# Optimization experiments

Measured on AMD Instinct MI355X. Metric: run time of the kernel, lower is better.

The kernel has to match this reference:

```python
import jax, jax.numpy as jnp
import numpy as np

B, L, D, H = 8, 1024, 1024, 16
DPH = D // H  # 64


def setup_inputs() -> dict:
    key = jax.random.key(0)
    ks = jax.random.split(key, 12)
    s = 1.0 / np.sqrt(D)
    return {
        "key": jax.random.normal(ks[0], (B, L, D), jnp.float32),
        "value": jax.random.normal(ks[1], (B, L, D), jnp.float32),
        "query": jax.random.normal(ks[2], (B, L, D), jnp.float32),
        "attn_mask": jax.random.randint(ks[3], (B, L, L), 0, 2) > 0,
        "Wq": jax.random.normal(ks[4], (D, D), jnp.float32) * s,
        "bq": jnp.zeros((D,), jnp.float32),
        "Wk": jax.random.normal(ks[5], (D, D), jnp.float32) * s,
        "bk": jnp.zeros((D,), jnp.float32),
        "Wv": jax.random.normal(ks[6], (D, D), jnp.float32) * s,
        "bv": jnp.zeros((D,), jnp.float32),
        "Wo": jax.random.normal(ks[7], (D, D), jnp.float32) * s,
        "bo": jnp.zeros((D,), jnp.float32),
        "gamma": jnp.ones((D,), jnp.float32),
        "beta": jnp.zeros((D,), jnp.float32),
    }


def _layer_norm(x, gamma, beta, eps=1e-5):
    mu = jnp.mean(x, axis=-1, keepdims=True)
    var = jnp.var(x, axis=-1, keepdims=True)
    return (x - mu) * jax.lax.rsqrt(var + eps) * gamma + beta


def reference(key, value, query, attn_mask, Wq, bq, Wk, bk, Wv, bv, Wo, bo, gamma, beta):
    residual = query
    k = key @ Wk + bk      # [B, L, D]
    v = value @ Wv + bv
    q = query @ Wq + bq
    # faithful to torch: raw row-major view into [B*H, L, dph] (NOT standard head transpose)
    k = k.reshape(B * H, -1, DPH)
    v = v.reshape(B * H, -1, DPH)
    q = q.reshape(B * H, -1, DPH)
    # faithful to torch repeat: tile whole batch H times along dim 0
    mask = jnp.tile(attn_mask, (H, 1, 1))  # [B*H, L, L]
    scale = DPH ** (-0.5)
    scores = jnp.einsum('bqd,bkd->bqk', q, k) * scale
    scores = jnp.where(mask, jnp.float32(-1e9), scores)
    attention = jax.nn.softmax(scores, axis=2)
    context = jnp.einsum('bqk,bkd->bqd', attention, v)  # [B*H, L, dph]
    context = context.reshape(B, -1, D)
    output = context @ Wo + bo
    output = _layer_norm(residual + output, gamma, beta)
    return (output, attention)
```

## Files before the change

kernel.cpp:

```cpp
#include <hip/hip_runtime.h>

typedef __attribute__((ext_vector_type(8))) short short8;
typedef __attribute__((ext_vector_type(4))) float f32x4;

#define AS1C(p) ((const __attribute__((address_space(1))) void*)(p))
#define AS3(p)  ((__attribute__((address_space(3))) void*)(p))

__device__ __forceinline__ unsigned short f2bf(float f) {
  unsigned int u = __float_as_uint(f);
  return (unsigned short)((u + 0x7fffu + ((u >> 16) & 1u)) >> 16);
}

__device__ __forceinline__ void gload16(const void* g, void* l) {
  __builtin_amdgcn_global_load_lds(AS1C(g), AS3(l), 16, 0, 0);
}

#define EXP_C 0.18033688011112042f

__global__ __launch_bounds__(256) void prep_kernel(const float* __restrict__ W0,
                                                   const float* __restrict__ W1,
                                                   const float* __restrict__ W2,
                                                   const float* __restrict__ W3,
                                                   unsigned short* __restrict__ WtBase,
                                                   const int* __restrict__ m,
                                                   unsigned int* __restrict__ bitsT,
                                                   const float* __restrict__ s0,
                                                   const float* __restrict__ s1,
                                                   const float* __restrict__ s2,
                                                   unsigned short* __restrict__ d0,
                                                   unsigned short* __restrict__ d1,
                                                   unsigned short* __restrict__ d2) {
  int bid = blockIdx.x;
  if (bid < 4096) {
    __shared__ float t[32][33];
    int z = bid >> 10;
    int rb = bid & 1023;
    int bx = (rb & 31) * 32, by = (rb >> 5) * 32;
    const float* W = (z == 0) ? W0 : (z == 1) ? W1 : (z == 2) ? W2 : W3;
    unsigned short* Wt = WtBase + (size_t)z * 1024 * 1024;
    int tx = threadIdx.x & 31, ty = threadIdx.x >> 5;
#pragma unroll
    for (int i = 0; i < 4; ++i) {
      int r = ty + i * 8;
      t[r][tx] = W[(size_t)(by + r) * 1024 + bx + tx];
    }
    __syncthreads();
#pragma unroll
    for (int i = 0; i < 4; ++i) {
      int r = ty + i * 8;
      Wt[(size_t)(bx + r) * 1024 + by + tx] = f2bf(t[tx][r]);
    }
  } else if (bid < 36864) {
    int i = (bid - 4096) * 256 + threadIdx.x;
    unsigned long long bl = __ballot(m[i] != 0);
    if ((threadIdx.x & 63) == 0) {
      int b_ = i >> 20, q = (i >> 10) & 1023, k = i & 1023;
      int w = k >> 5;
      bitsT[b_ * 32768 + w * 1024 + q]       = (unsigned int)bl;
      bitsT[b_ * 32768 + (w + 1) * 1024 + q] = (unsigned int)(bl >> 32);
    }
  } else {
    int cb = bid - 36864;
    int z = cb >> 13;
    const float* in = (z == 0) ? s0 : (z == 1) ? s1 : s2;
    unsigned short* out = (z == 0) ? d0 : (z == 1) ? d1 : d2;
    int i = (cb & 8191) * 256 + threadIdx.x;
    float4 v = ((const float4*)in)[i];
    ushort4 o;
    o.x = f2bf(v.x); o.y = f2bf(v.y); o.z = f2bf(v.z); o.w = f2bf(v.w);
    ((ushort4*)out)[i] = o;
  }
}

__global__ __launch_bounds__(256) void conv_bf16(const float* __restrict__ in,
                                                 unsigned short* __restrict__ out, int n4) {
  int i = blockIdx.x * 256 + threadIdx.x;
  if (i >= n4) return;
  float4 v = ((const float4*)in)[i];
  ushort4 o;
  o.x = f2bf(v.x); o.y = f2bf(v.y); o.z = f2bf(v.z); o.w = f2bf(v.w);
  ((ushort4*)out)[i] = o;
}

__global__ __launch_bounds__(256) void transpose_v(const unsigned short* __restrict__ v,
                                                   unsigned short* __restrict__ vt) {
  __shared__ unsigned short t[32][33];
  int b = blockIdx.z;
  int bx = blockIdx.x * 32;
  int by = blockIdx.y * 32;
  int tx = threadIdx.x & 31, ty = threadIdx.x >> 5;
#pragma unroll
  for (int i = 0; i < 4; ++i) {
    int r = ty + i * 8;
    t[r][tx] = v[(size_t)b * 65536 + (size_t)(by + r) * 64 + bx + tx];
  }
  __syncthreads();
#pragma unroll
  for (int i = 0; i < 4; ++i) {
    int r = ty + i * 8;
    vt[(size_t)b * 65536 + (size_t)(bx + r) * 1024 + by + tx] = t[tx][r];
  }
}

template <int MODE>
__device__ __forceinline__ void gemm_body(
    const unsigned short* __restrict__ A, const unsigned short* __restrict__ Bt,
    const float* __restrict__ bias, const float* __restrict__ res,
    unsigned short* __restrict__ Cb, float* __restrict__ Cf,
    unsigned short* lA, unsigned short* lB) {
  const int K = 1024, N = 1024;
  const int tid = threadIdx.x;
  const int wave = tid >> 6, lane = tid & 63;
  const int row_l = lane & 15, kg = lane >> 4;
  const int wg = blockIdx.y * 8 + blockIdx.x;
  const int idx = (wg & 7) * 64 + (wg >> 3);
  const int m0 = (idx >> 3) * 128, n0 = (idx & 7) * 128;
  const int wm = (wave >> 1) * 64, wn = (wave & 1) * 64;
  f32x4 acc[4][4] = {};

  for (int k0 = 0; k0 < K; k0 += 64) {
    __syncthreads();
#pragma unroll
    for (int it = 0; it < 4; ++it) {
      int c = wave * 64 + it * 256 + lane;
      int r = c >> 3, ch = c & 7;
      int sch = ch ^ (r & 7);
      gload16(A + (size_t)(m0 + r) * K + k0 + sch * 8, lA + (wave * 64 + it * 256) * 8);
      gload16(Bt + (size_t)(n0 + r) * K + k0 + sch * 8, lB + (wave * 64 + it * 256) * 8);
    }
    __syncthreads();
#pragma unroll
    for (int kk = 0; kk < 2; ++kk) {
      short8 af[4], bfr[4];
#pragma unroll
      for (int t = 0; t < 4; ++t) {
        int ra = wm + t * 16 + row_l;
        af[t] = *(const short8*)(lA + ra * 64 + (((kk * 4 + kg) ^ (ra & 7)) << 3));
        int rb = wn + t * 16 + row_l;
        bfr[t] = *(const short8*)(lB + rb * 64 + (((kk * 4 + kg) ^ (rb & 7)) << 3));
      }
      __builtin_amdgcn_s_setprio(1);
#pragma unroll
      for (int mt = 0; mt < 4; ++mt)
#pragma unroll
        for (int nt = 0; nt < 4; ++nt)
          acc[mt][nt] = __builtin_amdgcn_mfma_f32_16x16x32_bf16(af[mt], bfr[nt], acc[mt][nt], 0, 0, 0);
      __builtin_amdgcn_s_setprio(0);
    }
  }
#pragma unroll
  for (int mt = 0; mt < 4; ++mt)
#pragma unroll
    for (int nt = 0; nt < 4; ++nt)
#pragma unroll
      for (int r = 0; r < 4; ++r) {
        int grow = m0 + wm + mt * 16 + kg * 4 + r;
        int gcol = n0 + wn + nt * 16 + row_l;
        float v = acc[mt][nt][r] + bias[gcol];
        if (MODE == 0) {
          Cb[(size_t)grow * N + gcol] = f2bf(v);
        } else {
          v += res[(size_t)grow * N + gcol];
          Cf[(size_t)grow * N + gcol] = v;
        }
      }
}

__global__ __launch_bounds__(256) void gemm_qkv_kernel(
    const unsigned short* __restrict__ A0, const unsigned short* __restrict__ A1,
    const unsigned short* __restrict__ A2, const unsigned short* __restrict__ WtBase,
    const float* __restrict__ b0, const float* __restrict__ b1, const float* __restrict__ b2,
    unsigned short* __restrict__ C0, unsigned short* __restrict__ C1,
    unsigned short* __restrict__ C2) {
  __shared__ unsigned short lA[128 * 64];
  __shared__ unsigned short lB[128 * 64];
  int z = blockIdx.z;
  const unsigned short* A = (z == 0) ? A0 : (z == 1) ? A1 : A2;
  const float* bias = (z == 0) ? b0 : (z == 1) ? b1 : b2;
  unsigned short* C = (z == 0) ? C0 : (z == 1) ? C1 : C2;
  gemm_body<0>(A, WtBase + (size_t)z * 1024 * 1024, bias, nullptr, C, nullptr, lA, lB);
}

__global__ __launch_bounds__(256) void gemm_out_kernel(
    const unsigned short* __restrict__ A, const unsigned short* __restrict__ Bt,
    const float* __restrict__ bias, const float* __restrict__ res, float* __restrict__ Cf) {
  __shared__ unsigned short lA[128 * 64];
  __shared__ unsigned short lB[128 * 64];
  gemm_body<1>(A, Bt, bias, res, nullptr, Cf, lA, lB);
}

__global__ __launch_bounds__(256) void attn_kernel(
    const unsigned short* __restrict__ Q,
    const unsigned short* __restrict__ Km,
    const unsigned short* __restrict__ Vt,
    const unsigned int* __restrict__ mbitsT,
    float* __restrict__ attn,
    unsigned short* __restrict__ ctx) {
  __shared__ unsigned short lQ[64 * 64];
  __shared__ unsigned short lK[64 * 64];
  __shared__ unsigned short lV[64 * 64];
  const int tid = threadIdx.x, wave = tid >> 6, lane = tid & 63;
  const int row_l = lane & 15, kg = lane >> 4;
  const int wg = blockIdx.y * 16 + blockIdx.x;
  const int idx = (wg & 7) * 256 + (wg >> 3);
  const int batch = idx >> 4, qt = idx & 15;
  const int q0 = qt * 64;
  const unsigned short* Qb = Q + (size_t)batch * 65536;
  const unsigned short* Kb = Km + (size_t)batch * 65536;
  const unsigned short* Vb = Vt + (size_t)batch * 65536;
  const unsigned int* mT = mbitsT + (size_t)(batch & 7) * 32768;
  float* attb = attn + (size_t)batch * 1048576;
  const int q_loc = wave * 16 + row_l;
  const int q_lane = q0 + q_loc;

#define STAGE_K_TO(kt, dst)                                                           \
  {                                                                                   \
    _Pragma("unroll") for (int it = 0; it < 2; ++it) {                                \
      int c = wave * 64 + it * 256 + lane;                                            \
      int r_ = c >> 3, ch_ = c & 7, sch_ = ch_ ^ (r_ & 7);                            \
      gload16(Kb + (size_t)((kt) * 64 + r_) * 64 + sch_ * 8,                          \
              (dst) + (wave * 64 + it * 256) * 8);                                    \
    }                                                                                 \
  }
#define STAGE_V_TO(kt, dst)                                                           \
  {                                                                                   \
    _Pragma("unroll") for (int it = 0; it < 2; ++it) {                                \
      int c = wave * 64 + it * 256 + lane;                                            \
      int r_ = c >> 3, ch_ = c & 7, sch_ = ch_ ^ (r_ & 7);                            \
      gload16(Vb + (size_t)r_ * 1024 + (kt) * 64 + sch_ * 8,                          \
              (dst) + (wave * 64 + it * 256) * 8);                                    \
    }                                                                                 \
  }
#define WAIT_BAR0                                             \
  asm volatile("s_waitcnt vmcnt(0)" ::: "memory");            \
  __builtin_amdgcn_s_barrier();

#pragma unroll
  for (int it = 0; it < 2; ++it) {
    int c = wave * 64 + it * 256 + lane;
    int r = c >> 3, ch = c & 7;
    int sch = ch ^ (r & 7);
    gload16(Qb + (size_t)(q0 + r) * 64 + sch * 8, lQ + (wave * 64 + it * 256) * 8);
  }
  STAGE_K_TO(0, lK)
  WAIT_BAR0
  short8 qf[2];
#pragma unroll
  for (int kk = 0; kk < 2; ++kk)
    qf[kk] = *(const short8*)(lQ + q_loc * 64 + (((kk * 4 + kg) ^ (q_loc & 7)) << 3));

  float l_part = 0.f;

  auto pass1_step = [&](const unsigned short* kbuf, int kt) {
    unsigned int mw0 = mT[(kt * 2 + 0) * 1024 + q_lane];
    unsigned int mw1 = mT[(kt * 2 + 1) * 1024 + q_lane];
    f32x4 s[4];
    __builtin_amdgcn_s_setprio(1);
#pragma unroll
    for (int cf = 0; cf < 4; ++cf) {
      int rk = cf * 16 + row_l;
      f32x4 a = {0.f, 0.f, 0.f, 0.f};
#pragma unroll
      for (int kk = 0; kk < 2; ++kk) {
        short8 kf = *(const short8*)(kbuf + rk * 64 + (((kk * 4 + kg) ^ (rk & 7)) << 3));
        a = __builtin_amdgcn_mfma_f32_16x16x32_bf16(kf, qf[kk], a, 0, 0, 0);
      }
      s[cf] = a;
    }
    __builtin_amdgcn_s_setprio(0);
#pragma unroll
    for (int cf = 0; cf < 4; ++cf) {
      unsigned int w = (cf < 2) ? mw0 : mw1;
#pragma unroll
      for (int r = 0; r < 4; ++r) {
        int bit = (w >> ((cf & 1) * 16 + kg * 4 + r)) & 1;
        float e = __builtin_exp2f(s[cf][r] * EXP_C);
        l_part += bit ? 0.f : e;
      }
    }
  };
  for (int kt2 = 0; kt2 < 16; kt2 += 2) {
    STAGE_K_TO(kt2 + 1, lV)
    pass1_step(lK, kt2);
    WAIT_BAR0
    if (kt2 + 2 < 16) STAGE_K_TO(kt2 + 2, lK)
    pass1_step(lV, kt2 + 1);
    WAIT_BAR0
  }
  float se = l_part;
  se += __shfl_xor(se, 16);
  se += __shfl_xor(se, 32);
  const float il = 1.f / se;

  f32x4 cacc[4] = {};
  unsigned short* lP = lQ;

  for (int kt = 0; kt < 16; ++kt) {
    __syncthreads();
    STAGE_K_TO(kt, lK)
    STAGE_V_TO(kt, lV)
    WAIT_BAR0
    unsigned int mw0 = mT[(kt * 2 + 0) * 1024 + q_lane];
    unsigned int mw1 = mT[(kt * 2 + 1) * 1024 + q_lane];
    f32x4 s[4];
    __builtin_amdgcn_s_setprio(1);
#pragma unroll
    for (int cf = 0; cf < 4; ++cf) {
      int rk = cf * 16 + row_l;
      f32x4 a = {0.f, 0.f, 0.f, 0.f};
#pragma unroll
      for (int kk = 0; kk < 2; ++kk) {
        short8 kf = *(const short8*)(lK + rk * 64 + (((kk * 4 + kg) ^ (rk & 7)) << 3));
        a = __builtin_amdgcn_mfma_f32_16x16x32_bf16(kf, qf[kk], a, 0, 0, 0);
      }
      s[cf] = a;
    }
    __builtin_amdgcn_s_setprio(0);
#pragma unroll
    for (int cf = 0; cf < 4; ++cf) {
      unsigned int w = (cf < 2) ? mw0 : mw1;
      f32x4 o;
      unsigned short pb[4];
#pragma unroll
      for (int r = 0; r < 4; ++r) {
        int bit = (w >> ((cf & 1) * 16 + kg * 4 + r)) & 1;
        float p = bit ? 0.f : __builtin_exp2f(s[cf][r] * EXP_C) * il;
        o[r] = p;
        pb[r] = f2bf(p);
      }
      int swc = (cf * 2 + (kg >> 1)) ^ (q_loc & 7);
      *(uint2*)((char*)lP + q_loc * 128 + swc * 16 + (kg & 1) * 8) = *(const uint2*)pb;
      __builtin_nontemporal_store(
          o, (f32x4*)(attb + (size_t)q_lane * 1024 + kt * 64 + cf * 16 + kg * 4));
    }
    __builtin_amdgcn_s_setprio(1);
#pragma unroll
    for (int kk = 0; kk < 2; ++kk) {
      short8 pa = *(const short8*)(lP + q_loc * 64 + (((kk * 4 + kg) ^ (q_loc & 7)) << 3));
#pragma unroll
      for (int df = 0; df < 4; ++df) {
        int rv = df * 16 + row_l;
        short8 vb = *(const short8*)(lV + rv * 64 + (((kk * 4 + kg) ^ (rv & 7)) << 3));
        cacc[df] = __builtin_amdgcn_mfma_f32_16x16x32_bf16(pa, vb, cacc[df], 0, 0, 0);
      }
    }
    __builtin_amdgcn_s_setprio(0);
  }
#pragma unroll
  for (int df = 0; df < 4; ++df)
#pragma unroll
    for (int r = 0; r < 4; ++r) {
      int grow = q0 + wave * 16 + kg * 4 + r;
      int gcol = df * 16 + row_l;
      ctx[(size_t)batch * 65536 + (size_t)grow * 64 + gcol] = f2bf(cacc[df][r]);
    }
#undef STAGE_K_TO
#undef STAGE_V_TO
#undef WAIT_BAR0
}

__global__ __launch_bounds__(256) void layernorm_kernel(float* __restrict__ io,
                                                        const float* __restrict__ gamma,
                                                        const float* __restrict__ beta) {
  int wave = threadIdx.x >> 6, lane = threadIdx.x & 63;
  size_t row = (size_t)blockIdx.x * 4 + wave;
  float* p = io + row * 1024;
  float4 v[4];
  float s = 0.f, ss = 0.f;
#pragma unroll
  for (int i = 0; i < 4; ++i) {
    v[i] = ((const float4*)p)[lane + i * 64];
    s += v[i].x + v[i].y + v[i].z + v[i].w;
    ss += v[i].x * v[i].x + v[i].y * v[i].y + v[i].z * v[i].z + v[i].w * v[i].w;
  }
#pragma unroll
  for (int m = 1; m < 64; m <<= 1) { s += __shfl_xor(s, m); ss += __shfl_xor(ss, m); }
  float mu = s * (1.f / 1024.f);
  float var = ss * (1.f / 1024.f) - mu * mu;
  float rinv = rsqrtf(var + 1e-5f);
#pragma unroll
  for (int i = 0; i < 4; ++i) {
    int idx = lane + i * 64;
    float4 g = ((const float4*)gamma)[idx];
    float4 b = ((const float4*)beta)[idx];
    float4 o;
    o.x = (v[i].x - mu) * rinv * g.x + b.x;
    o.y = (v[i].y - mu) * rinv * g.y + b.y;
    o.z = (v[i].z - mu) * rinv * g.z + b.z;
    o.w = (v[i].w - mu) * rinv * g.w + b.w;
    ((float4*)p)[idx] = o;
  }
}

extern "C" void kernel_launch(void* const* d_in, const int* in_sizes, int n_in,
                              void* d_out, int out_size, void* d_ws, size_t ws_size,
                              hipStream_t stream) {
  const float* key   = (const float*)d_in[0];
  const float* value = (const float*)d_in[1];
  const float* query = (const float*)d_in[2];
  const int* amask   = (const int*)d_in[3];
  const float* Wq = (const float*)d_in[4];
  const float* bq = (const float*)d_in[5];
  const float* Wk = (const float*)d_in[6];
  const float* bk = (const float*)d_in[7];
  const float* Wv = (const float*)d_in[8];
  const float* bv = (const float*)d_in[9];
  const float* Wo = (const float*)d_in[10];
  const float* bo = (const float*)d_in[11];
  const float* gamma = (const float*)d_in[12];
  const float* beta  = (const float*)d_in[13];

  char* ws = (char*)d_ws;
  const size_t MB = 1024 * 1024;
  float* out_f = (float*)d_out;
  float* attn_f = (float*)d_out + (size_t)8388608;
  const int n4 = 8388608 / 4;
  dim3 gemm_grid(8, 64);
  dim3 gemm_grid3(8, 64, 3);
  dim3 attn_grid(16, 128);

  const bool big_ws = ws_size >= 106 * MB;
  if (big_ws) {
    unsigned short* A0 = (unsigned short*)(ws + 0);
    unsigned short* A1 = (unsigned short*)(ws + 16 * MB);
    unsigned short* A2 = (unsigned short*)(ws + 32 * MB);
    unsigned short* B1 = (unsigned short*)(ws + 48 * MB);
    unsigned short* B2 = (unsigned short*)(ws + 64 * MB);
    unsigned short* B3 = (unsigned short*)(ws + 80 * MB);
    unsigned short* Wts = (unsigned short*)(ws + 96 * MB);
    unsigned int* mbitsT = (unsigned int*)(ws + 104 * MB);

    prep_kernel<<<61440, 256, 0, stream>>>(Wq, Wk, Wv, Wo, Wts, amask, mbitsT,
                                           query, key, value, A0, A1, A2);
    gemm_qkv_kernel<<<gemm_grid3, 256, 0, stream>>>(A0, A1, A2, Wts, bq, bk, bv, B1, B2, B3);
    transpose_v<<<dim3(2, 32, 128), 256, 0, stream>>>(B3, A1);
    attn_kernel<<<attn_grid, 256, 0, stream>>>(B1, B2, A1, mbitsT, attn_f, A2);
    gemm_out_kernel<<<gemm_grid, 256, 0, stream>>>(A2, Wts + 3 * MB, bo, query, out_f);
    layernorm_kernel<<<2048, 256, 0, stream>>>(out_f, gamma, beta);
  } else {
    unsigned short* B0 = (unsigned short*)(ws + 0);
    unsigned short* B1 = (unsigned short*)(ws + 16 * MB);
    unsigned short* B2 = (unsigned short*)(ws + 32 * MB);
    unsigned short* B3 = (unsigned short*)(ws + 48 * MB);
    unsigned short* Wts = (unsigned short*)(ws + 64 * MB);
    unsigned int* mbitsT = (unsigned int*)(ws + 72 * MB);

    prep_kernel<<<36864, 256, 0, stream>>>(Wq, Wk, Wv, Wo, Wts, amask, mbitsT,
                                           query, key, value, B0, B0, B0);
    conv_bf16<<<8192, 256, 0, stream>>>(query, B0, n4);
    gemm_qkv_kernel<<<gemm_grid, 256, 0, stream>>>(B0, B0, B0, Wts, bq, bq, bq, B1, B1, B1);
    conv_bf16<<<8192, 256, 0, stream>>>(key, B0, n4);
    gemm_qkv_kernel<<<gemm_grid, 256, 0, stream>>>(B0, B0, B0, Wts + 1 * MB, bk, bk, bk, B2, B2, B2);
    conv_bf16<<<8192, 256, 0, stream>>>(value, B0, n4);
    gemm_qkv_kernel<<<gemm_grid, 256, 0, stream>>>(B0, B0, B0, Wts + 2 * MB, bv, bv, bv, B3, B3, B3);
    transpose_v<<<dim3(2, 32, 128), 256, 0, stream>>>(B3, B0);
    attn_kernel<<<attn_grid, 256, 0, stream>>>(B1, B2, B0, mbitsT, attn_f, B3);
    gemm_out_kernel<<<gemm_grid, 256, 0, stream>>>(B3, Wts + 3 * MB, bo, query, out_f);
    layernorm_kernel<<<2048, 256, 0, stream>>>(out_f, gamma, beta);
  }
}
```

Before: 321.6 us.

## Process two query tiles per attention block, fusing tile B's row-sum pass into tile A's output pass

Each attention workgroup now handles 128 queries as two 64-row sub-tiles that share the same K/V staging, and the grid is halved to match. The row-sum pass for sub-tile B runs inside sub-tile A's output loop, so K is streamed three times per 128 queries instead of four. The pass-1 K loop also loses its double buffering, and the block runs half as many workgroups with more registers live. That may hurt latency hiding and occupancy in exchange for less global K/V traffic.

```diff
diff --git a/kernel.cpp b/kernel.cpp
--- a/kernel.cpp
+++ b/kernel.cpp
@@ -196,22 +196,23 @@
     const unsigned int* __restrict__ mbitsT,
     float* __restrict__ attn,
     unsigned short* __restrict__ ctx) {
-  __shared__ unsigned short lQ[64 * 64];
+  __shared__ unsigned short lQ[128 * 64];
   __shared__ unsigned short lK[64 * 64];
   __shared__ unsigned short lV[64 * 64];
   const int tid = threadIdx.x, wave = tid >> 6, lane = tid & 63;
   const int row_l = lane & 15, kg = lane >> 4;
-  const int wg = blockIdx.y * 16 + blockIdx.x;
-  const int idx = (wg & 7) * 256 + (wg >> 3);
-  const int batch = idx >> 4, qt = idx & 15;
-  const int q0 = qt * 64;
+  const int wg = blockIdx.y * 8 + blockIdx.x;
+  const int idx = (wg & 7) * 128 + (wg >> 3);
+  const int batch = idx >> 3, qt2 = idx & 7;
+  const int q0 = qt2 * 128;
   const unsigned short* Qb = Q + (size_t)batch * 65536;
   const unsigned short* Kb = Km + (size_t)batch * 65536;
   const unsigned short* Vb = Vt + (size_t)batch * 65536;
   const unsigned int* mT = mbitsT + (size_t)(batch & 7) * 32768;
   float* attb = attn + (size_t)batch * 1048576;
   const int q_loc = wave * 16 + row_l;
-  const int q_lane = q0 + q_loc;
+  const int qA = q0 + q_loc;
+  const int qB = q0 + 64 + q_loc;
 
 #define STAGE_K_TO(kt, dst)                                                           \
   {                                                                                   \
@@ -235,8 +236,23 @@
   asm volatile("s_waitcnt vmcnt(0)" ::: "memory");            \
   __builtin_amdgcn_s_barrier();
 
-#pragma unroll
-  for (int it = 0; it < 2; ++it) {
+#define QKT(sdst, kbuf, qfrag)                                                        \
+  {                                                                                   \
+    __builtin_amdgcn_s_setprio(1);                                                    \
+    _Pragma("unroll") for (int cf = 0; cf < 4; ++cf) {                                \
+      int rk = cf * 16 + row_l;                                                       \
+      f32x4 a_ = {0.f, 0.f, 0.f, 0.f};                                                \
+      _Pragma("unroll") for (int kk = 0; kk < 2; ++kk) {                              \
+        short8 kf = *(const short8*)((kbuf) + rk * 64 + (((kk * 4 + kg) ^ (rk & 7)) << 3)); \
+        a_ = __builtin_amdgcn_mfma_f32_16x16x32_bf16(kf, (qfrag)[kk], a_, 0, 0, 0);   \
+      }                                                                               \
+      (sdst)[cf] = a_;                                                                \
+    }                                                                                 \
+    __builtin_amdgcn_s_setprio(0);                                                    \
+  }
+
+#pragma unroll
+  for (int it = 0; it < 4; ++it) {
     int c = wave * 64 + it * 256 + lane;
     int r = c >> 3, ch = c & 7;
     int sch = ch ^ (r & 7);
@@ -244,30 +260,20 @@
   }
   STAGE_K_TO(0, lK)
   WAIT_BAR0
-  short8 qf[2];
-#pragma unroll
-  for (int kk = 0; kk < 2; ++kk)
-    qf[kk] = *(const short8*)(lQ + q_loc * 64 + (((kk * 4 + kg) ^ (q_loc & 7)) << 3));
-
-  float l_part = 0.f;
-
-  auto pass1_step = [&](const unsigned short* kbuf, int kt) {
-    unsigned int mw0 = mT[(kt * 2 + 0) * 1024 + q_lane];
-    unsigned int mw1 = mT[(kt * 2 + 1) * 1024 + q_lane];
+  short8 qfA[2], qfB[2];
+#pragma unroll
+  for (int kk = 0; kk < 2; ++kk) {
+    qfA[kk] = *(const short8*)(lQ + q_loc * 64 + (((kk * 4 + kg) ^ (q_loc & 7)) << 3));
+    int rB = 64 + q_loc;
+    qfB[kk] = *(const short8*)(lQ + rB * 64 + (((kk * 4 + kg) ^ (rB & 7)) << 3));
+  }
+
+  float l_partA = 0.f;
+  for (int kt = 0; kt < 16; ++kt) {
+    unsigned int mw0 = mT[(kt * 2 + 0) * 1024 + qA];
+    unsigned int mw1 = mT[(kt * 2 + 1) * 1024 + qA];
     f32x4 s[4];
-    __builtin_amdgcn_s_setprio(1);
-#pragma unroll
-    for (int cf = 0; cf < 4; ++cf) {
-      int rk = cf * 16 + row_l;
-      f32x4 a = {0.f, 0.f, 0.f, 0.f};
-#pragma unroll
-      for (int kk = 0; kk < 2; ++kk) {
-        short8 kf = *(const short8*)(kbuf + rk * 64 + (((kk * 4 + kg) ^ (rk & 7)) << 3));
-        a = __builtin_amdgcn_mfma_f32_16x16x32_bf16(kf, qf[kk], a, 0, 0, 0);
-      }
-      s[cf] = a;
-    }
-    __builtin_amdgcn_s_setprio(0);
+    QKT(s, lK, qfA)
 #pragma unroll
     for (int cf = 0; cf < 4; ++cf) {
       unsigned int w = (cf < 2) ? mw0 : mw1;
@@ -275,47 +281,97 @@
       for (int r = 0; r < 4; ++r) {
         int bit = (w >> ((cf & 1) * 16 + kg * 4 + r)) & 1;
         float e = __builtin_exp2f(s[cf][r] * EXP_C);
-        l_part += bit ? 0.f : e;
-      }
-    }
-  };
-  for (int kt2 = 0; kt2 < 16; kt2 += 2) {
-    STAGE_K_TO(kt2 + 1, lV)
-    pass1_step(lK, kt2);
-    WAIT_BAR0
-    if (kt2 + 2 < 16) STAGE_K_TO(kt2 + 2, lK)
-    pass1_step(lV, kt2 + 1);
-    WAIT_BAR0
-  }
-  float se = l_part;
-  se += __shfl_xor(se, 16);
-  se += __shfl_xor(se, 32);
-  const float il = 1.f / se;
-
-  f32x4 cacc[4] = {};
-  unsigned short* lP = lQ;
+        l_partA += bit ? 0.f : e;
+      }
+    }
+    __syncthreads();
+    if (kt < 15) {
+      STAGE_K_TO(kt + 1, lK)
+      WAIT_BAR0
+    }
+  }
+  float seA = l_partA;
+  seA += __shfl_xor(seA, 16);
+  seA += __shfl_xor(seA, 32);
+  const float ilA = 1.f / seA;
+
+  unsigned short* lPA = lQ;
+  unsigned short* lPB = lQ + 64 * 64;
+  f32x4 caccA[4] = {};
+  f32x4 caccB[4] = {};
+  float l_partB = 0.f;
 
   for (int kt = 0; kt < 16; ++kt) {
     __syncthreads();
     STAGE_K_TO(kt, lK)
     STAGE_V_TO(kt, lV)
+    unsigned int mwA0 = mT[(kt * 2 + 0) * 1024 + qA];
+    unsigned int mwA1 = mT[(kt * 2 + 1) * 1024 + qA];
+    unsigned int mwB0 = mT[(kt * 2 + 0) * 1024 + qB];
+    unsigned int mwB1 = mT[(kt * 2 + 1) * 1024 + qB];
     WAIT_BAR0
-    unsigned int mw0 = mT[(kt * 2 + 0) * 1024 + q_lane];
-    unsigned int mw1 = mT[(kt * 2 + 1) * 1024 + q_lane];
+    {
+      f32x4 s[4];
+      QKT(s, lK, qfB)
+#pragma unroll
+      for (int cf = 0; cf < 4; ++cf) {
+        unsigned int w = (cf < 2) ? mwB0 : mwB1;
+#pragma unroll
+        for (int r = 0; r < 4; ++r) {
+          int bit = (w >> ((cf & 1) * 16 + kg * 4 + r)) & 1;
+          float e = __builtin_exp2f(s[cf][r] * EXP_C);
+          l_partB += bit ? 0.f : e;
+        }
+      }
+    }
+    {
+      f32x4 s[4];
+      QKT(s, lK, qfA)
+#pragma unroll
+      for (int cf = 0; cf < 4; ++cf) {
+        unsigned int w = (cf < 2) ? mwA0 : mwA1;
+        f32x4 o;
+        unsigned short pb[4];
+#pragma unroll
+        for (int r = 0; r < 4; ++r) {
+          int bit = (w >> ((cf & 1) * 16 + kg * 4 + r)) & 1;
+          float p = bit ? 0.f : __builtin_exp2f(s[cf][r] * EXP_C) * ilA;
+          o[r] = p;
+          pb[r] = f2bf(p);
+        }
+        int swc = (cf * 2 + (kg >> 1)) ^ (q_loc & 7);
+        *(uint2*)((char*)lPA + q_loc * 128 + swc * 16 + (kg & 1) * 8) = *(const uint2*)pb;
+        __builtin_nontemporal_store(
+            o, (f32x4*)(attb + (size_t)qA * 1024 + kt * 64 + cf * 16 + kg * 4));
+      }
+      __builtin_amdgcn_s_setprio(1);
+#pragma unroll
+      for (int kk = 0; kk < 2; ++kk) {
+        short8 pa = *(const short8*)(lPA + q_loc * 64 + (((kk * 4 + kg) ^ (q_loc & 7)) << 3));
+#pragma unroll
+        for (int df = 0; df < 4; ++df) {
+          int rv = df * 16 + row_l;
+          short8 vb = *(const short8*)(lV + rv * 64 + (((kk * 4 + kg) ^ (rv & 7)) << 3));
+          caccA[df] = __builtin_amdgcn_mfma_f32_16x16x32_bf16(pa, vb, caccA[df], 0, 0, 0);
+        }
+      }
+      __builtin_amdgcn_s_setprio(0);
+    }
+  }
+  float seB = l_partB;
+  seB += __shfl_xor(seB, 16);
+  seB += __shfl_xor(seB, 32);
+  const float ilB = 1.f / seB;
+
+  for (int kt = 0; kt < 16; ++kt) {
+    __syncthreads();
+    STAGE_K_TO(kt, lK)
+    STAGE_V_TO(kt, lV)
+    unsigned int mw0 = mT[(kt * 2 + 0) * 1024 + qB];
+    unsigned int mw1 = mT[(kt * 2 + 1) * 1024 + qB];
+    WAIT_BAR0
     f32x4 s[4];
-    __builtin_amdgcn_s_setprio(1);
-#pragma unroll
-    for (int cf = 0; cf < 4; ++cf) {
-      int rk = cf * 16 + row_l;
-      f32x4 a = {0.f, 0.f, 0.f, 0.f};
-#pragma unroll
-      for (int kk = 0; kk < 2; ++kk) {
-        short8 kf = *(const short8*)(lK + rk * 64 + (((kk * 4 + kg) ^ (rk & 7)) << 3));
-        a = __builtin_amdgcn_mfma_f32_16x16x32_bf16(kf, qf[kk], a, 0, 0, 0);
-      }
-      s[cf] = a;
-    }
-    __builtin_amdgcn_s_setprio(0);
+    QKT(s, lK, qfB)
 #pragma unroll
     for (int cf = 0; cf < 4; ++cf) {
       unsigned int w = (cf < 2) ? mw0 : mw1;
@@ -324,24 +380,24 @@
 #pragma unroll
       for (int r = 0; r < 4; ++r) {
         int bit = (w >> ((cf & 1) * 16 + kg * 4 + r)) & 1;
-        float p = bit ? 0.f : __builtin_exp2f(s[cf][r] * EXP_C) * il;
+        float p = bit ? 0.f : __builtin_exp2f(s[cf][r] * EXP_C) * ilB;
         o[r] = p;
         pb[r] = f2bf(p);
       }
       int swc = (cf * 2 + (kg >> 1)) ^ (q_loc & 7);
-      *(uint2*)((char*)lP + q_loc * 128 + swc * 16 + (kg & 1) * 8) = *(const uint2*)pb;
+      *(uint2*)((char*)lPB + q_loc * 128 + swc * 16 + (kg & 1) * 8) = *(const uint2*)pb;
       __builtin_nontemporal_store(
-          o, (f32x4*)(attb + (size_t)q_lane * 1024 + kt * 64 + cf * 16 + kg * 4));
+          o, (f32x4*)(attb + (size_t)qB * 1024 + kt * 64 + cf * 16 + kg * 4));
     }
     __builtin_amdgcn_s_setprio(1);
 #pragma unroll
     for (int kk = 0; kk < 2; ++kk) {
-      short8 pa = *(const short8*)(lP + q_loc * 64 + (((kk * 4 + kg) ^ (q_loc & 7)) << 3));
+      short8 pa = *(const short8*)(lPB + q_loc * 64 + (((kk * 4 + kg) ^ (q_loc & 7)) << 3));
 #pragma unroll
       for (int df = 0; df < 4; ++df) {
         int rv = df * 16 + row_l;
         short8 vb = *(const short8*)(lV + rv * 64 + (((kk * 4 + kg) ^ (rv & 7)) << 3));
-        cacc[df] = __builtin_amdgcn_mfma_f32_16x16x32_bf16(pa, vb, cacc[df], 0, 0, 0);
+        caccB[df] = __builtin_amdgcn_mfma_f32_16x16x32_bf16(pa, vb, caccB[df], 0, 0, 0);
       }
     }
     __builtin_amdgcn_s_setprio(0);
@@ -350,13 +406,15 @@
   for (int df = 0; df < 4; ++df)
 #pragma unroll
     for (int r = 0; r < 4; ++r) {
-      int grow = q0 + wave * 16 + kg * 4 + r;
+      int rowA = q0 + wave * 16 + kg * 4 + r;
       int gcol = df * 16 + row_l;
-      ctx[(size_t)batch * 65536 + (size_t)grow * 64 + gcol] = f2bf(cacc[df][r]);
+      ctx[(size_t)batch * 65536 + (size_t)rowA * 64 + gcol] = f2bf(caccA[df][r]);
+      ctx[(size_t)batch * 65536 + (size_t)(rowA + 64) * 64 + gcol] = f2bf(caccB[df][r]);
     }
 #undef STAGE_K_TO
 #undef STAGE_V_TO
 #undef WAIT_BAR0
+#undef QKT
 }
 
 __global__ __launch_bounds__(256) void layernorm_kernel(float* __restrict__ io,
@@ -417,7 +475,7 @@
   const int n4 = 8388608 / 4;
   dim3 gemm_grid(8, 64);
   dim3 gemm_grid3(8, 64, 3);
-  dim3 attn_grid(16, 128);
+  dim3 attn_grid(8, 128);
 
   const bool big_ws = ws_size >= 106 * MB;
   if (big_ws) {
```

Result: slower. 427.9 us (+33.1%).
